# Kernel optimization log

Measured on AMD Instinct MI355X. Metric: run time of the kernel, lower is better.

## Reference

```python
import math
import jax, jax.numpy as jnp
import numpy as np

B, N, DIM, H = 2, 4096, 1024, 16
DH = DIM // H
LEVELS = int(math.log2(N))
SCALE = 1.0 / math.sqrt(DH)


def build_lookup_table(seq_len):
    """Replicates build_hierarchical_index_lookup_table (numpy, static)."""
    levels = int(math.log2(seq_len))
    total_nodes = 2 * seq_len - 1
    max_valid = total_nodes - 2
    idx = np.full((seq_len, levels), -1, dtype=np.int32)
    cm = np.zeros((seq_len, levels), dtype=bool)
    for n in range(seq_len):
        nc = n
        for l in range(levels):
            if l == 0:
                pair = nc
                nn = nc ^ 1
            else:
                pair = nc // 2 + seq_len
                nn = pair ^ 1  # (nc//2 + seq_len) ^ 1 per Python precedence
            if nn > max_valid:
                break
            if pair < nn:
                cm[n, l] = True  # neighbor is to the right -> causally masked
            idx[n, l] = nn
            nc = nn
    return idx, cm


def setup_inputs() -> dict:
    key = jax.random.key(0)
    ks = jax.random.split(key, 12)
    w = lambda k: (jax.random.normal(k, (DIM, DIM), dtype=jnp.float32) * 0.02)
    idx_np, cm_np = build_lookup_table(N)
    return {
        "x": jax.random.normal(ks[0], (B, N, DIM), dtype=jnp.float32),
        "Wq_y": w(ks[1]), "Wk_y": w(ks[2]), "Wv_y": w(ks[3]),
        "Wo_y": w(ks[4]), "bo_y": jnp.zeros((DIM,), jnp.float32),
        "Wq_x": w(ks[5]), "Wk_x": w(ks[6]), "Wv_x": w(ks[7]),
        "Wo_x": w(ks[8]), "bo_x": jnp.zeros((DIM,), jnp.float32),
        "idx_map": jnp.asarray(idx_np, dtype=jnp.int32),       # [N, LEVELS]
        "causal_mask": jnp.asarray(cm_np, dtype=jnp.bool_),    # [N, LEVELS]
    }


def _heads(t):
    b, n, _ = t.shape
    return t.reshape(b, n, H, DH)


def _forward(x, Wq_y, Wk_y, Wv_y, Wo_y, bo_y, Wq_x, Wk_x, Wv_x, Wo_x, bo_x,
             idx_map, causal_mask):
    # ---- stage 1: build parent nodes level by level (online 2-child softmax merge)
    nodes = [x]  # leaves: [B, N, DIM]; parents appended level by level
    cur = x
    for _ in range(LEVELS):
        pre = 0.5 * (cur[:, 0::2] + cur[:, 1::2])     # parent query source [B,P,DIM]
        q = _heads(pre @ Wq_y)                        # [B,P,H,DH]
        k = _heads(cur @ Wk_y)                        # [B,C,H,DH]
        v = _heads(cur @ Wv_y)
        s0 = jnp.einsum('bphd,bphd->bph', q, k[:, 0::2]) * SCALE
        s1 = jnp.einsum('bphd,bphd->bph', q, k[:, 1::2]) * SCALE
        m = jnp.maximum(s0, s1)
        e0 = jnp.exp(s0 - m)
        e1 = jnp.exp(s1 - m)
        denom = e0 + e1 + 1e-9
        parent = ((e0 / denom)[..., None] * v[:, 0::2]
                  + (e1 / denom)[..., None] * v[:, 1::2])   # [B,P,H,DH]
        bp, pp = parent.shape[0], parent.shape[1]
        parent = parent.reshape(bp, pp, DIM) @ Wo_y + bo_y
        nodes.append(parent)
        cur = parent
    h_all = jnp.concatenate(nodes, axis=1)            # [B, 2N-1, DIM]

    # ---- stage 2: fused multi-level gather attention over self + neighbors
    Q = _heads(x @ Wq_x)                              # leaf queries [B,N,H,DH]
    K_all = _heads(h_all @ Wk_x)                      # [B,2N-1,H,DH]
    V_all = _heads(h_all @ Wv_x)

    k_cross = jnp.take(K_all, idx_map, axis=1)        # [B,N,LEVELS,H,DH]
    v_cross = jnp.take(V_all, idx_map, axis=1)

    s_self = jnp.einsum('bnhd,bnhd->bnh', Q, K_all[:, :N]) * SCALE   # [B,N,H]
    s_cross = jnp.einsum('bnhd,bnlhd->bnhl', Q, k_cross) * SCALE     # [B,N,H,L]
    neg_inf = jnp.float32(-jnp.inf)
    s_cross = jnp.where(causal_mask[None, :, None, :], neg_inf, s_cross)

    scores = jnp.concatenate([s_self[..., None], s_cross], axis=-1)  # [B,N,H,L+1]
    w = jax.nn.softmax(scores, axis=-1)
    out = (w[..., 0:1] * V_all[:, :N]
           + jnp.einsum('bnhl,bnlhd->bnhd', w[..., 1:], v_cross))    # [B,N,H,DH]
    return out.reshape(B, N, DIM) @ Wo_x + bo_x


def reference(x, Wq_y, Wk_y, Wv_y, Wo_y, bo_y, Wq_x, Wk_x, Wv_x, Wo_x, bo_x,
              idx_map, causal_mask):
    return _forward(x, Wq_y, Wk_y, Wv_y, Wo_y, bo_y,
                    Wq_x, Wk_x, Wv_x, Wo_x, bo_x, idx_map, causal_mask)
```

## Files before the change

kernel.cpp:

```cpp
#include <hip/hip_runtime.h>
#include <stdint.h>

#define H_NODES 8191
#define NN 4096
#define DIMC 1024

typedef __bf16 bf16x8 __attribute__((ext_vector_type(8)));
typedef float f32x4 __attribute__((ext_vector_type(4)));

__device__ __forceinline__ float b2f(ushort u) {
  union { uint32_t i; float f; } x; x.i = ((uint32_t)u) << 16; return x.f;
}
__device__ __forceinline__ ushort f2b(float f) {
  union { float f; uint32_t i; } x; x.f = f;
  uint32_t r = x.i + 0x7FFFu + ((x.i >> 16) & 1u);
  return (ushort)(r >> 16);
}
__device__ __forceinline__ void load16f(const ushort* p, float* f) {
  const uint32_t* w = (const uint32_t*)p;
  #pragma unroll
  for (int i = 0; i < 8; ++i) {
    uint32_t v = w[i];
    f[2 * i]     = b2f((ushort)(v & 0xffff));
    f[2 * i + 1] = b2f((ushort)(v >> 16));
  }
}
__device__ __forceinline__ void store16b(ushort* p, const float* f) {
  uint32_t w[8];
  #pragma unroll
  for (int i = 0; i < 8; ++i)
    w[i] = (uint32_t)f2b(f[2 * i]) | ((uint32_t)f2b(f[2 * i + 1]) << 16);
  *(uint4*)p = *(const uint4*)&w[0];
  *(uint4*)(p + 8) = *(const uint4*)&w[4];
}

struct WPtrs { const float* w[8]; };

__global__ void __launch_bounds__(256) transpose_w_k(WPtrs wp, ushort* __restrict__ dst) {
  __shared__ float t[32][33];
  const float* src = wp.w[blockIdx.z];
  int c0 = blockIdx.x * 32, r0 = blockIdx.y * 32;
  int tx = threadIdx.x, ty = threadIdx.y;
  #pragma unroll
  for (int i = ty; i < 32; i += 8)
    t[i][tx] = src[(long)(r0 + i) * DIMC + c0 + tx];
  __syncthreads();
  ushort* d = dst + (long)blockIdx.z * DIMC * DIMC;
  #pragma unroll
  for (int i = ty; i < 32; i += 8)
    d[(long)(c0 + i) * DIMC + r0 + tx] = f2b(t[tx][i]);
}

__global__ void __launch_bounds__(256) cvt_x_k(const float* __restrict__ x, ushort* __restrict__ h) {
  long t = (long)blockIdx.x * 256 + threadIdx.x;
  long i = t << 2;
  if (i >= (long)2 * NN * DIMC) return;
  long row = i >> 10;
  int col = (int)(i & 1023);
  long b = row >> 12;
  long n = row & 4095;
  float4 v = *(const float4*)(x + i);
  ushort* d = h + ((b * H_NODES + n) << 10) + col;
  uint2 pk;
  pk.x = (uint32_t)f2b(v.x) | ((uint32_t)f2b(v.y) << 16);
  pk.y = (uint32_t)f2b(v.z) | ((uint32_t)f2b(v.w) << 16);
  *(uint2*)d = pk;
}

__global__ void __launch_bounds__(256) avg_pairs_k(const ushort* __restrict__ h,
    ushort* __restrict__ pre, int P, int offL) {
  long t = (long)blockIdx.x * 256 + threadIdx.x;
  if (t >= (long)2 * P * 128) return;
  int dblk = (int)(t & 127);
  long r = t >> 7;
  int b = (r >= P) ? 1 : 0;
  int p = (int)(r - (long)b * P);
  const ushort* c = h + (((long)(b * H_NODES + offL + 2 * p)) << 10) + dblk * 8;
  const uint4 a0 = *(const uint4*)c;
  const uint4 a1 = *(const uint4*)(c + DIMC);
  const uint32_t* pa = (const uint32_t*)&a0;
  const uint32_t* pb = (const uint32_t*)&a1;
  uint32_t outw[4];
  #pragma unroll
  for (int i = 0; i < 4; ++i) {
    float x0 = b2f((ushort)(pa[i] & 0xffff)), x1 = b2f((ushort)(pa[i] >> 16));
    float y0 = b2f((ushort)(pb[i] & 0xffff)), y1 = b2f((ushort)(pb[i] >> 16));
    ushort r0 = f2b(0.5f * (x0 + y0)), r1 = f2b(0.5f * (x1 + y1));
    outw[i] = (uint32_t)r0 | ((uint32_t)r1 << 16);
  }
  *(uint4*)(pre + (((long)(b * P + p)) << 10) + dblk * 8) = *(const uint4*)outw;
}

struct GemmDesc {
  const ushort* A; long sAb;
  const ushort* Bt;
  const float* bias;
  void* C; long sCb; int ldc;
  int M; int outMode;
  int tX, tY;
  ushort* preC;
  long sPreB;
};

__device__ __forceinline__ void stage_tile(const GemmDesc& d, const ushort* Ab,
    int row0, int col0, ushort* lA, ushort* lB, int kt, int wave, int lane) {
  #pragma unroll
  for (int j = 0; j < 4; ++j) {
    int s = wave * 256 + j * 64 + lane;
    int r = s >> 3, slot = s & 7;
    int gb = slot ^ (r & 7);
    int gr = row0 + r; gr = (gr < d.M) ? gr : (d.M - 1);
    const ushort* srcA = Ab + (long)gr * DIMC + kt * 64 + gb * 8;
    __builtin_amdgcn_global_load_lds(
        (const __attribute__((address_space(1))) void*)(uintptr_t)srcA,
        (__attribute__((address_space(3))) void*)(uint32_t)(uintptr_t)(lA + s * 8),
        16, 0, 0);
    const ushort* srcB = d.Bt + (long)(col0 + r) * DIMC + kt * 64 + gb * 8;
    __builtin_amdgcn_global_load_lds(
        (const __attribute__((address_space(1))) void*)(uintptr_t)srcB,
        (__attribute__((address_space(3))) void*)(uint32_t)(uintptr_t)(lB + s * 8),
        16, 0, 0);
  }
}

__device__ __forceinline__ void gemm_tile(const GemmDesc& d, int bz, int row0, int col0,
    ushort (*lA)[8192], ushort (*lB)[8192], int tid) {
  const ushort* Ab = d.A + (long)bz * d.sAb;
  int wave = tid >> 6, lane = tid & 63;
  int wr = wave >> 1, wc = wave & 1;

  f32x4 acc[4][4];
  #pragma unroll
  for (int m = 0; m < 4; ++m)
    #pragma unroll
    for (int n = 0; n < 4; ++n) acc[m][n] = (f32x4){0.f, 0.f, 0.f, 0.f};

  stage_tile(d, Ab, row0, col0, lA[0], lB[0], 0, wave, lane);

  int rr = lane & 15, g4 = lane >> 4;
  for (int kt = 0; kt < 16; ++kt) {
    int cur = kt & 1;
    if (kt + 1 < 16) {
      stage_tile(d, Ab, row0, col0, lA[cur ^ 1], lB[cur ^ 1], kt + 1, wave, lane);
      asm volatile("s_waitcnt vmcnt(8)" ::: "memory");
    } else {
      asm volatile("s_waitcnt vmcnt(0)" ::: "memory");
    }
    __builtin_amdgcn_s_barrier();
    #pragma unroll
    for (int ks = 0; ks < 2; ++ks) {
      bf16x8 af[4], bfr[4];
      #pragma unroll
      for (int m = 0; m < 4; ++m) {
        int r = wr * 64 + m * 16 + rr;
        int slot = (ks * 4 + g4) ^ (r & 7);
        af[m] = *reinterpret_cast<const bf16x8*>(&lA[cur][r * 64 + slot * 8]);
      }
      #pragma unroll
      for (int n = 0; n < 4; ++n) {
        int r = wc * 64 + n * 16 + rr;
        int slot = (ks * 4 + g4) ^ (r & 7);
        bfr[n] = *reinterpret_cast<const bf16x8*>(&lB[cur][r * 64 + slot * 8]);
      }
      __builtin_amdgcn_s_setprio(1);
      #pragma unroll
      for (int m = 0; m < 4; ++m)
        #pragma unroll
        for (int n = 0; n < 4; ++n)
          acc[m][n] = __builtin_amdgcn_mfma_f32_16x16x32_bf16(af[m], bfr[n], acc[m][n], 0, 0, 0);
      __builtin_amdgcn_s_setprio(0);
    }
    __builtin_amdgcn_s_barrier();
  }

  int rq = lane >> 4;
  #pragma unroll
  for (int n = 0; n < 4; ++n) {
    int col = col0 + wc * 64 + n * 16 + rr;
    float bv = d.bias ? d.bias[col] : 0.0f;
    #pragma unroll
    for (int m = 0; m < 4; ++m) {
      int gr0 = row0 + wr * 64 + m * 16 + rq * 4;
      float vv[4];
      #pragma unroll
      for (int r = 0; r < 4; ++r) vv[r] = acc[m][n][r] + bv;
      #pragma unroll
      for (int r = 0; r < 4; ++r) {
        int gr = gr0 + r;
        if (gr < d.M) {
          long o = (long)bz * d.sCb + (long)gr * d.ldc + col;
          if (d.outMode == 2) ((float*)d.C)[o] = vv[r];
          else ((ushort*)d.C)[o] = f2b(vv[r]);
        }
      }
      if (d.preC) {
        #pragma unroll
        for (int r = 0; r < 4; r += 2) {
          int gr = gr0 + r;
          if (gr + 1 < d.M)
            d.preC[(long)bz * d.sPreB + (long)(gr >> 1) * DIMC + col] =
                f2b(0.5f * (vv[r] + vv[r + 1]));
        }
      }
    }
  }
}

__global__ void __launch_bounds__(256) gemm_multi(GemmDesc d0, GemmDesc d1, int t0) {
  __shared__ __align__(16) ushort lA[2][8192];
  __shared__ __align__(16) ushort lB[2][8192];
  int t = blockIdx.x;
  const GemmDesc& d = (t < t0) ? d0 : d1;
  int u = (t < t0) ? t : t - t0;
  int per = d.tX * d.tY;
  int bz = u / per;
  int rem = u - bz * per;
  int ty = rem / d.tX;
  int tx = rem - ty * d.tX;
  gemm_tile(d, bz, tx * 128, ty * 128, lA, lB, threadIdx.x);
}

__global__ void __launch_bounds__(256) merge_y2_k(const ushort* __restrict__ q,
    const ushort* __restrict__ kv, ushort* __restrict__ outp, int P) {
  int wave = threadIdx.x >> 6, lane = threadIdx.x & 63;
  long w = (long)blockIdx.x * 4 + wave;
  if (w >= (long)2 * P) return;
  int b = (w >= P) ? 1 : 0;
  int p = (int)(w - (long)b * P);
  const ushort* qp = q + (((long)(b * P + p)) << 10) + lane * 16;
  const ushort* kvb = kv + ((long)(b * 2 * P + 2 * p)) * 2048;
  float qf[16], k0f[16], k1f[16];
  load16f(qp, qf);
  load16f(kvb + lane * 16, k0f);
  load16f(kvb + 2048 + lane * 16, k1f);
  float d0 = 0.f, d1 = 0.f;
  #pragma unroll
  for (int j = 0; j < 16; ++j) { d0 += qf[j] * k0f[j]; d1 += qf[j] * k1f[j]; }
  d0 += __shfl_xor(d0, 1); d0 += __shfl_xor(d0, 2);
  d1 += __shfl_xor(d1, 1); d1 += __shfl_xor(d1, 2);
  float s0 = d0 * 0.125f, s1 = d1 * 0.125f;
  float mm = fmaxf(s0, s1);
  float e0 = expf(s0 - mm), e1 = expf(s1 - mm);
  float inv = 1.0f / (e0 + e1 + 1e-9f);
  float w0 = e0 * inv, w1 = e1 * inv;
  float v0f[16], v1f[16], ov[16];
  load16f(kvb + 1024 + lane * 16, v0f);
  load16f(kvb + 2048 + 1024 + lane * 16, v1f);
  #pragma unroll
  for (int j = 0; j < 16; ++j) ov[j] = w0 * v0f[j] + w1 * v1f[j];
  store16b(outp + (((long)(b * P + p)) << 10) + lane * 16, ov);
}

__global__ void __launch_bounds__(256) attn_x2_k(const ushort* __restrict__ Q,
    const ushort* __restrict__ KV, ushort* __restrict__ outp) {
  int wave = threadIdx.x >> 6, lane = threadIdx.x & 63;
  long w = (long)blockIdx.x * 4 + wave;
  int n = (int)(w & 4095);
  int b = (int)(w >> 12);
  const ushort* KVb = KV + (long)b * H_NODES * 2048;
  float qf[16];
  load16f(Q + (((long)b * NN + n) << 10) + lane * 16, qf);
  int nb[13];
  nb[0] = n;
  #pragma unroll
  for (int l = 0; l < 12; ++l) nb[1 + l] = (8192 - (8192 >> l)) + ((n >> l) ^ 1);
  float s[13];
  #pragma unroll
  for (int i = 0; i < 13; ++i) {
    float kf[16];
    load16f(KVb + (long)nb[i] * 2048 + lane * 16, kf);
    float d = 0.f;
    #pragma unroll
    for (int j = 0; j < 16; ++j) d += qf[j] * kf[j];
    d += __shfl_xor(d, 1);
    d += __shfl_xor(d, 2);
    s[i] = d * 0.125f;
  }
  #pragma unroll
  for (int l = 0; l < 12; ++l)
    if (((n >> l) & 1) == 0) s[1 + l] = -__builtin_inff();
  float mm = s[0];
  #pragma unroll
  for (int i = 1; i < 13; ++i) mm = fmaxf(mm, s[i]);
  float e[13], sum = 0.f;
  #pragma unroll
  for (int i = 0; i < 13; ++i) { e[i] = expf(s[i] - mm); sum += e[i]; }
  float inv = 1.0f / sum;
  float ov[16];
  #pragma unroll
  for (int j = 0; j < 16; ++j) ov[j] = 0.f;
  #pragma unroll
  for (int i = 0; i < 13; ++i) {
    float wgt = e[i] * inv;
    float vf[16];
    load16f(KVb + (long)nb[i] * 2048 + 1024 + lane * 16, vf);
    #pragma unroll
    for (int j = 0; j < 16; ++j) ov[j] += wgt * vf[j];
  }
  store16b(outp + (((long)b * NN + n) << 10) + lane * 16, ov);
}

extern "C" void kernel_launch(void* const* d_in, const int* in_sizes, int n_in,
                              void* d_out, int out_size, void* d_ws, size_t ws_size,
                              hipStream_t stream) {
  const float* x    = (const float*)d_in[0];
  const float* Wq_y = (const float*)d_in[1];
  const float* Wk_y = (const float*)d_in[2];
  const float* Wv_y = (const float*)d_in[3];
  const float* Wo_y = (const float*)d_in[4];
  const float* bo_y = (const float*)d_in[5];
  const float* Wq_x = (const float*)d_in[6];
  const float* Wk_x = (const float*)d_in[7];
  const float* Wv_x = (const float*)d_in[8];
  const float* Wo_x = (const float*)d_in[9];
  const float* bo_x = (const float*)d_in[10];

  ushort* wt  = (ushort*)d_ws;
  ushort* h   = wt + (size_t)8 * 1024 * 1024;
  ushort* reg = h + (size_t)2 * H_NODES * DIMC;
  ushort* Qx   = reg;
  ushort* KVa  = Qx + (size_t)2 * 4096 * DIMC;
  ushort* aout = KVa + (size_t)2 * H_NODES * 2048;
  ushort* preB = aout;
  ushort* qbB  = preB + (size_t)2 * 2048 * DIMC;
  ushort* kv1B = qbB + (size_t)2 * 2048 * DIMC;
  ushort* mrgB = kv1B + (size_t)2 * 4096 * 2048;
  ushort* preS = preB;
  ushort* qbS  = qbB;
  ushort* kv1S = kv1B;
  ushort* mrgS = mrgB;

  size_t wsElems = (size_t)8 * 1024 * 1024 + (size_t)2 * H_NODES * DIMC +
                   (size_t)2 * 4096 * DIMC + (size_t)2 * H_NODES * 2048 +
                   ((size_t)2 * 2048 * DIMC * 2 + (size_t)2 * 4096 * 2048 +
                    (size_t)2 * 2048 * DIMC);
  if (ws_size < wsElems * 2) return;

  WPtrs wp;
  wp.w[0] = Wq_y; wp.w[1] = Wk_y; wp.w[2] = Wv_y; wp.w[3] = Wo_y;
  wp.w[4] = Wq_x; wp.w[5] = Wk_x; wp.w[6] = Wv_x; wp.w[7] = Wo_x;
  transpose_w_k<<<dim3(32, 32, 8), dim3(32, 8), 0, stream>>>(wp, wt);
  cvt_x_k<<<8192, 256, 0, stream>>>(x, h);
  avg_pairs_k<<<(2 * 2048 * 128 + 255) / 256, 256, 0, stream>>>(h, preB, 2048, 0);

  auto mk128 = [](const ushort* A, long sAb, const ushort* Bt, const float* bias,
                  void* C, long sCb, int ldc, int M, int outMode, int tY) {
    GemmDesc d; d.A = A; d.sAb = sAb; d.Bt = Bt; d.bias = bias; d.C = C; d.sCb = sCb;
    d.ldc = ldc; d.M = M; d.outMode = outMode; d.tX = (M + 127) / 128; d.tY = tY;
    d.preC = nullptr; d.sPreB = 0;
    return d;
  };
  auto kvSub = [&](long start, int len) {
    return mk128(h + start * DIMC, (long)H_NODES * DIMC, wt + (size_t)5 * 1024 * 1024,
                 nullptr, KVa + start * 2048, (long)H_NODES * 2048, 2048, len, 0, 16);
  };
  auto qSub = [&](long start, int len) {
    return mk128(h + start * DIMC, (long)H_NODES * DIMC, wt + (size_t)4 * 1024 * 1024,
                 nullptr, Qx + start * DIMC, (long)4096 * DIMC, DIMC, len, 0, 8);
  };

  for (int l = 0; l < 12; ++l) {
    int P = NN >> (l + 1);
    int offL = 8192 - (8192 >> l);
    int offP = 8192 - (8192 >> (l + 1));
    ushort* pre = (l >= 3) ? preS : preB;
    ushort* qb  = (l >= 3) ? qbS  : qbB;
    ushort* kv1 = (l >= 3) ? kv1S : kv1B;
    ushort* mrg = (l >= 3) ? mrgS : mrgB;

    GemmDesc dq  = mk128(pre, (long)P * DIMC, wt, nullptr,
                         qb, (long)P * DIMC, DIMC, P, 0, 8);
    GemmDesc dkv = mk128(h + (long)offL * DIMC, (long)H_NODES * DIMC,
                         wt + (size_t)1 * 1024 * 1024, nullptr,
                         kv1, (long)2 * P * 2048, 2048, 2 * P, 0, 16);
    int t0 = dq.tX * dq.tY * 2;
    gemm_multi<<<t0 + dkv.tX * dkv.tY * 2, 256, 0, stream>>>(dq, dkv, t0);

    merge_y2_k<<<(2 * P + 3) / 4, 256, 0, stream>>>(qb, kv1, mrg, P);

    GemmDesc dgo = mk128(mrg, (long)P * DIMC, wt + (size_t)3 * 1024 * 1024, bo_y,
                         h + (long)offP * DIMC, (long)H_NODES * DIMC, DIMC, P, 1, 8);
    if (l < 11) {
      dgo.preC = (l >= 2) ? preS : preB;
      dgo.sPreB = (long)(P / 2) * DIMC;
    }
    GemmDesc att = dgo; int nAtt = 0;
    if      (l == 0)  att = qSub(0, 2048);
    else if (l == 1)  att = qSub(2048, 2048);
    else if (l == 2)  att = kvSub(0, 1792);
    else if (l == 3)  att = kvSub(1792, 1920);
    else if (l == 4)  att = kvSub(3712, 1920);
    else if (l == 5)  att = kvSub(5632, 1536);
    else if (l == 6)  att = kvSub(7168, 512);
    else if (l == 7)  att = kvSub(7680, 256);
    else if (l == 8)  att = kvSub(7936, 128);
    else if (l == 9)  att = kvSub(8064, 64);
    else if (l == 10) att = kvSub(8128, 32);
    else if (l == 11) att = kvSub(8160, 16);
    nAtt = att.tX * att.tY * 2;
    int n0 = dgo.tX * dgo.tY * 2;
    gemm_multi<<<n0 + nAtt, 256, 0, stream>>>(dgo, att, n0);
  }

  {
    GemmDesc a0 = kvSub(8176, 8), a1 = kvSub(8184, 7);
    int n0 = a0.tX * a0.tY * 2, n1 = a1.tX * a1.tY * 2;
    gemm_multi<<<n0 + n1, 256, 0, stream>>>(a0, a1, n0);
  }
  attn_x2_k<<<2048, 256, 0, stream>>>(Qx, KVa, aout);
  {
    GemmDesc dox = mk128(aout, (long)4096 * DIMC, wt + (size_t)7 * 1024 * 1024, bo_x,
                         d_out, (long)4096 * DIMC, DIMC, 4096, 2, 8);
    gemm_multi<<<dox.tX * dox.tY * 2, 256, 0, stream>>>(dox, dox, dox.tX * dox.tY * 2);
  }
}
```

Baseline: 697.5 us.

## Split GEMM K dimension across two wave groups with LDS reduction

```diff
diff --git a/kernel.cpp b/kernel.cpp
--- a/kernel.cpp
+++ b/kernel.cpp
@@ -103,19 +103,19 @@
 };
 
 __device__ __forceinline__ void stage_tile(const GemmDesc& d, const ushort* Ab,
-    int row0, int col0, ushort* lA, ushort* lB, int kt, int wave, int lane) {
-  #pragma unroll
-  for (int j = 0; j < 4; ++j) {
-    int s = wave * 256 + j * 64 + lane;
-    int r = s >> 3, slot = s & 7;
-    int gb = slot ^ (r & 7);
+    int row0, int col0, ushort* lA, ushort* lB, int ktG, int wg, int lane) {
+  #pragma unroll
+  for (int j = 0; j < 2; ++j) {
+    int s = wg * 128 + j * 64 + lane;
+    int r = s >> 2;
+    int g = (s & 3) ^ ((r >> 1) & 3);
     int gr = row0 + r; gr = (gr < d.M) ? gr : (d.M - 1);
-    const ushort* srcA = Ab + (long)gr * DIMC + kt * 64 + gb * 8;
+    const ushort* srcA = Ab + (long)gr * DIMC + ktG * 32 + g * 8;
     __builtin_amdgcn_global_load_lds(
         (const __attribute__((address_space(1))) void*)(uintptr_t)srcA,
         (__attribute__((address_space(3))) void*)(uint32_t)(uintptr_t)(lA + s * 8),
         16, 0, 0);
-    const ushort* srcB = d.Bt + (long)(col0 + r) * DIMC + kt * 64 + gb * 8;
+    const ushort* srcB = d.Bt + (long)(col0 + r) * DIMC + ktG * 32 + g * 8;
     __builtin_amdgcn_global_load_lds(
         (const __attribute__((address_space(1))) void*)(uintptr_t)srcB,
         (__attribute__((address_space(3))) void*)(uint32_t)(uintptr_t)(lB + s * 8),
@@ -124,10 +124,15 @@
 }
 
 __device__ __forceinline__ void gemm_tile(const GemmDesc& d, int bz, int row0, int col0,
-    ushort (*lA)[8192], ushort (*lB)[8192], int tid) {
+    ushort* smem, int tid) {
   const ushort* Ab = d.A + (long)bz * d.sAb;
   int wave = tid >> 6, lane = tid & 63;
-  int wr = wave >> 1, wc = wave & 1;
+  int grp = wave >> 2, wg = wave & 3;
+  int wr = wg >> 1, wc = wg & 1;
+  ushort* aB0 = smem + (grp * 2) * 4096;
+  ushort* aB1 = smem + (grp * 2 + 1) * 4096;
+  ushort* bB0 = smem + 16384 + (grp * 2) * 4096;
+  ushort* bB1 = smem + 16384 + (grp * 2 + 1) * 4096;
 
   f32x4 acc[4][4];
   #pragma unroll
@@ -135,43 +140,63 @@
     #pragma unroll
     for (int n = 0; n < 4; ++n) acc[m][n] = (f32x4){0.f, 0.f, 0.f, 0.f};
 
-  stage_tile(d, Ab, row0, col0, lA[0], lB[0], 0, wave, lane);
+  stage_tile(d, Ab, row0, col0, aB0, bB0, grp * 16, wg, lane);
 
   int rr = lane & 15, g4 = lane >> 4;
   for (int kt = 0; kt < 16; ++kt) {
-    int cur = kt & 1;
+    ushort* aCur = (kt & 1) ? aB1 : aB0;
+    ushort* bCur = (kt & 1) ? bB1 : bB0;
     if (kt + 1 < 16) {
-      stage_tile(d, Ab, row0, col0, lA[cur ^ 1], lB[cur ^ 1], kt + 1, wave, lane);
-      asm volatile("s_waitcnt vmcnt(8)" ::: "memory");
+      ushort* aNxt = (kt & 1) ? aB0 : aB1;
+      ushort* bNxt = (kt & 1) ? bB0 : bB1;
+      stage_tile(d, Ab, row0, col0, aNxt, bNxt, grp * 16 + kt + 1, wg, lane);
+      asm volatile("s_waitcnt vmcnt(4)" ::: "memory");
     } else {
       asm volatile("s_waitcnt vmcnt(0)" ::: "memory");
     }
     __builtin_amdgcn_s_barrier();
-    #pragma unroll
-    for (int ks = 0; ks < 2; ++ks) {
-      bf16x8 af[4], bfr[4];
+    bf16x8 af[4], bfr[4];
+    #pragma unroll
+    for (int m = 0; m < 4; ++m) {
+      int r = wr * 64 + m * 16 + rr;
+      int slot = g4 ^ ((r >> 1) & 3);
+      af[m] = *reinterpret_cast<const bf16x8*>(&aCur[r * 32 + slot * 8]);
+    }
+    #pragma unroll
+    for (int n = 0; n < 4; ++n) {
+      int r = wc * 64 + n * 16 + rr;
+      int slot = g4 ^ ((r >> 1) & 3);
+      bfr[n] = *reinterpret_cast<const bf16x8*>(&bCur[r * 32 + slot * 8]);
+    }
+    __builtin_amdgcn_s_setprio(1);
+    #pragma unroll
+    for (int m = 0; m < 4; ++m)
       #pragma unroll
-      for (int m = 0; m < 4; ++m) {
-        int r = wr * 64 + m * 16 + rr;
-        int slot = (ks * 4 + g4) ^ (r & 7);
-        af[m] = *reinterpret_cast<const bf16x8*>(&lA[cur][r * 64 + slot * 8]);
-      }
+      for (int n = 0; n < 4; ++n)
+        acc[m][n] = __builtin_amdgcn_mfma_f32_16x16x32_bf16(af[m], bfr[n], acc[m][n], 0, 0, 0);
+    __builtin_amdgcn_s_setprio(0);
+    __builtin_amdgcn_s_barrier();
+  }
+
+  __builtin_amdgcn_s_barrier();
+  f32x4* red = (f32x4*)smem;
+  if (grp == 1) {
+    int q = tid - 256;
+    #pragma unroll
+    for (int m = 0; m < 4; ++m)
       #pragma unroll
-      for (int n = 0; n < 4; ++n) {
-        int r = wc * 64 + n * 16 + rr;
-        int slot = (ks * 4 + g4) ^ (r & 7);
-        bfr[n] = *reinterpret_cast<const bf16x8*>(&lB[cur][r * 64 + slot * 8]);
-      }
-      __builtin_amdgcn_s_setprio(1);
-      #pragma unroll
-      for (int m = 0; m < 4; ++m)
-        #pragma unroll
-        for (int n = 0; n < 4; ++n)
-          acc[m][n] = __builtin_amdgcn_mfma_f32_16x16x32_bf16(af[m], bfr[n], acc[m][n], 0, 0, 0);
-      __builtin_amdgcn_s_setprio(0);
-    }
-    __builtin_amdgcn_s_barrier();
-  }
+      for (int n = 0; n < 4; ++n)
+        red[(m * 4 + n) * 256 + q] = acc[m][n];
+  }
+  __builtin_amdgcn_s_barrier();
+  asm volatile("s_waitcnt lgkmcnt(0)" ::: "memory");
+  if (grp != 0) return;
+
+  #pragma unroll
+  for (int m = 0; m < 4; ++m)
+    #pragma unroll
+    for (int n = 0; n < 4; ++n)
+      acc[m][n] += red[(m * 4 + n) * 256 + tid];
 
   int rq = lane >> 4;
   #pragma unroll
@@ -206,9 +231,8 @@
   }
 }
 
-__global__ void __launch_bounds__(256) gemm_multi(GemmDesc d0, GemmDesc d1, int t0) {
-  __shared__ __align__(16) ushort lA[2][8192];
-  __shared__ __align__(16) ushort lB[2][8192];
+__global__ void __launch_bounds__(512) gemm_multi(GemmDesc d0, GemmDesc d1, int t0) {
+  __shared__ __align__(16) ushort smem[32768];
   int t = blockIdx.x;
   const GemmDesc& d = (t < t0) ? d0 : d1;
   int u = (t < t0) ? t : t - t0;
@@ -217,7 +241,7 @@
   int rem = u - bz * per;
   int ty = rem / d.tX;
   int tx = rem - ty * d.tX;
-  gemm_tile(d, bz, tx * 128, ty * 128, lA, lB, threadIdx.x);
+  gemm_tile(d, bz, tx * 128, ty * 128, smem, threadIdx.x);
 }
 
 __global__ void __launch_bounds__(256) merge_y2_k(const ushort* __restrict__ q,
@@ -374,7 +398,7 @@
                          wt + (size_t)1 * 1024 * 1024, nullptr,
                          kv1, (long)2 * P * 2048, 2048, 2 * P, 0, 16);
     int t0 = dq.tX * dq.tY * 2;
-    gemm_multi<<<t0 + dkv.tX * dkv.tY * 2, 256, 0, stream>>>(dq, dkv, t0);
+    gemm_multi<<<t0 + dkv.tX * dkv.tY * 2, 512, 0, stream>>>(dq, dkv, t0);
 
     merge_y2_k<<<(2 * P + 3) / 4, 256, 0, stream>>>(qb, kv1, mrg, P);
 
@@ -399,18 +423,18 @@
     else if (l == 11) att = kvSub(8160, 16);
     nAtt = att.tX * att.tY * 2;
     int n0 = dgo.tX * dgo.tY * 2;
-    gemm_multi<<<n0 + nAtt, 256, 0, stream>>>(dgo, att, n0);
+    gemm_multi<<<n0 + nAtt, 512, 0, stream>>>(dgo, att, n0);
   }
 
   {
     GemmDesc a0 = kvSub(8176, 8), a1 = kvSub(8184, 7);
     int n0 = a0.tX * a0.tY * 2, n1 = a1.tX * a1.tY * 2;
-    gemm_multi<<<n0 + n1, 256, 0, stream>>>(a0, a1, n0);
+    gemm_multi<<<n0 + n1, 512, 0, stream>>>(a0, a1, n0);
   }
   attn_x2_k<<<2048, 256, 0, stream>>>(Qx, KVa, aout);
   {
     GemmDesc dox = mk128(aout, (long)4096 * DIMC, wt + (size_t)7 * 1024 * 1024, bo_x,
                          d_out, (long)4096 * DIMC, DIMC, 4096, 2, 8);
-    gemm_multi<<<dox.tX * dox.tY * 2, 256, 0, stream>>>(dox, dox, dox.tX * dox.tY * 2);
-  }
-}
+    gemm_multi<<<dox.tX * dox.tY * 2, 512, 0, stream>>>(dox, dox, dox.tX * dox.tY * 2);
+  }
+}
```

Measured after the change: 671.4 us. 3.7% less time.
